# Kernel tuning notes

Hardware: AMD Instinct MI355X
Metric: run time of the kernel (lower is better)

Reference implementation:

```python
import jax, jax.numpy as jnp
import numpy as np

B, N, K = 2, 8192, 16
C_IN, C_OUT = 32, 64
EPS = 1e-6


def _bn(x, g, b, axes):
    m = jnp.mean(x, axes, keepdims=True)
    v = jnp.var(x, axes, keepdims=True)
    return (x - m) * jax.lax.rsqrt(v + EPS) * g + b


def _leaky(x, s):
    return jnp.where(x >= 0, x, s * x)


def _knn(coords, k):
    # brute-force euclidean KNN, self point included (dist 0)
    sq = jnp.sum(coords * coords, -1)  # (B,N)
    d2 = sq[:, :, None] + sq[:, None, :] - 2.0 * jnp.einsum('bnd,bmd->bnm', coords, coords)
    neg, idx = jax.lax.top_k(-d2, k)  # (B,N,K)
    dist = jnp.sqrt(jnp.clip(-neg, 1e-12, None))
    return idx, dist


def setup_inputs() -> dict:
    key = jax.random.key(0)
    ks = jax.random.split(key, 12)
    h = C_OUT // 2
    w = lambda k, s: jax.random.normal(k, s, jnp.float32) * 0.05
    return {
        'coords': jax.random.normal(ks[0], (B, N, 3), jnp.float32),
        'features': jax.random.normal(ks[1], (B, N, C_IN), jnp.float32),
        'W_mlp1': w(ks[2], (C_IN, h)), 'b_mlp1': jnp.zeros(h, jnp.float32),
        'W_lse1': w(ks[3], (10, h)), 'b_lse1': jnp.zeros(h, jnp.float32),
        'g_lse1': jnp.ones(h, jnp.float32), 'be_lse1': jnp.zeros(h, jnp.float32),
        'W_att1_lin': w(ks[4], (C_OUT, C_OUT)),
        'W_att1_mlp': w(ks[5], (C_OUT, h)), 'b_att1_mlp': jnp.zeros(h, jnp.float32),
        'g_att1': jnp.ones(h, jnp.float32), 'be_att1': jnp.zeros(h, jnp.float32),
        'W_lse2': w(ks[6], (10, h)), 'b_lse2': jnp.zeros(h, jnp.float32),
        'g_lse2': jnp.ones(h, jnp.float32), 'be_lse2': jnp.zeros(h, jnp.float32),
        'W_att2_lin': w(ks[7], (C_OUT, C_OUT)),
        'W_att2_mlp': w(ks[8], (C_OUT, C_OUT)), 'b_att2_mlp': jnp.zeros(C_OUT, jnp.float32),
        'g_att2': jnp.ones(C_OUT, jnp.float32), 'be_att2': jnp.zeros(C_OUT, jnp.float32),
        'W_mlp2': w(ks[9], (C_OUT, 2 * C_OUT)), 'b_mlp2': jnp.zeros(2 * C_OUT, jnp.float32),
        'W_short': w(ks[10], (C_IN, 2 * C_OUT)), 'b_short': jnp.zeros(2 * C_OUT, jnp.float32),
        'g_short': jnp.ones(2 * C_OUT, jnp.float32), 'be_short': jnp.zeros(2 * C_OUT, jnp.float32),
    }


def _forward(coords, features, W_mlp1, b_mlp1, W_lse1, b_lse1, g_lse1, be_lse1,
             W_att1_lin, W_att1_mlp, b_att1_mlp, g_att1, be_att1,
             W_lse2, b_lse2, g_lse2, be_lse2,
             W_att2_lin, W_att2_mlp, b_att2_mlp, g_att2, be_att2,
             W_mlp2, b_mlp2, W_short, b_short, g_short, be_short):
    idx, dist = _knn(coords, K)                     # (B,N,K)
    nbr = jax.vmap(lambda c, i: c[i])(coords, idx)  # gather neighbor coords (B,N,K,3)
    center = jnp.broadcast_to(coords[:, :, None, :], nbr.shape)
    # spatial encoding: [center, neighbor, center-neighbor, dist] -> 10 channels
    se = jnp.concatenate([center, nbr, center - nbr, dist[..., None]], -1)  # (B,N,K,10)

    # mlp1 (1x1 conv + LeakyReLU(0.2)), no BN
    x = _leaky(features @ W_mlp1 + b_mlp1, 0.2)     # (B,N,h)

    # LocSE 1: shared MLP (BN train-mode + ReLU) on spatial enc, concat features
    sp1 = jax.nn.relu(_bn(se @ W_lse1 + b_lse1, g_lse1, be_lse1, (0, 1, 2)))  # (B,N,K,h)
    x1 = jnp.concatenate([sp1, jnp.broadcast_to(x[:, :, None, :], sp1.shape)], -1)  # (B,N,K,2h)

    # attention pooling 1: softmax over neighbors K, weighted sum, MLP+BN+ReLU
    sc1 = jax.nn.softmax(x1 @ W_att1_lin, axis=2)
    p1 = jnp.sum(sc1 * x1, axis=2)                  # (B,N,2h)
    x = jax.nn.relu(_bn(p1 @ W_att1_mlp + b_att1_mlp, g_att1, be_att1, (0, 1)))  # (B,N,h)

    # LocSE 2 + attention pooling 2 (same KNN, separate weights)
    sp2 = jax.nn.relu(_bn(se @ W_lse2 + b_lse2, g_lse2, be_lse2, (0, 1, 2)))
    x2 = jnp.concatenate([sp2, jnp.broadcast_to(x[:, :, None, :], sp2.shape)], -1)
    sc2 = jax.nn.softmax(x2 @ W_att2_lin, axis=2)
    p2 = jnp.sum(sc2 * x2, axis=2)
    x = jax.nn.relu(_bn(p2 @ W_att2_mlp + b_att2_mlp, g_att2, be_att2, (0, 1)))  # (B,N,C_OUT)

    # mlp2 (no BN, no act) + shortcut (BN, no act), residual LeakyReLU(0.01)
    x = x @ W_mlp2 + b_mlp2                          # (B,N,2*C_OUT)
    short = _bn(features @ W_short + b_short, g_short, be_short, (0, 1))
    out = _leaky(x + short, 0.01)
    # match torch layout (B, 2*C_OUT, N, 1)
    return jnp.transpose(out, (0, 2, 1))[..., None]


def reference(coords, features, W_mlp1, b_mlp1, W_lse1, b_lse1, g_lse1, be_lse1,
              W_att1_lin, W_att1_mlp, b_att1_mlp, g_att1, be_att1,
              W_lse2, b_lse2, g_lse2, be_lse2,
              W_att2_lin, W_att2_mlp, b_att2_mlp, g_att2, be_att2,
              W_mlp2, b_mlp2, W_short, b_short, g_short, be_short):
    return _forward(coords, features, W_mlp1, b_mlp1, W_lse1, b_lse1, g_lse1, be_lse1,
                    W_att1_lin, W_att1_mlp, b_att1_mlp, g_att1, be_att1,
                    W_lse2, b_lse2, g_lse2, be_lse2,
                    W_att2_lin, W_att2_mlp, b_att2_mlp, g_att2, be_att2,
                    W_mlp2, b_mlp2, W_short, b_short, g_short, be_short)
```

## Files before the change

### kernel.cpp

```cpp
#include <hip/hip_runtime.h>
#include <cfloat>
#include <cmath>

#define DEV __device__ __forceinline__

constexpr int BB = 2, NN = 8192, KK = 16, CIN = 32, HH = 32, CO = 64, C2 = 128;
constexpr int BNTOT = BB * NN;
constexpr int BNKROWS = BB * NN * KK;
constexpr float EPSF = 1e-6f;
constexpr int NCELL = 4096;
constexpr int CAP = 128;

constexpr int S_LSE1 = 0, S_LSE2 = 64, S_ATT1 = 128, S_ATT2 = 192, S_SHORT = 320, S_TOTAL = 576;

constexpr size_t OFF_CP4   = 0;
constexpr size_t OFF_SE    = OFF_CP4 + (size_t)BNTOT * 4;
constexpr size_t OFF_XF    = OFF_SE + (size_t)BNKROWS * 10;
constexpr size_t OFF_SHORT = OFF_XF + (size_t)BNTOT * HH;
constexpr size_t OFF_PRE1  = OFF_SHORT + (size_t)BNTOT * C2;
constexpr size_t OFF_PRE2  = OFF_PRE1 + (size_t)BNTOT * HH;
constexpr size_t OFF_STATS = OFF_PRE2 + (size_t)BNTOT * CO;
constexpr size_t OFF_COUNTS= OFF_STATS + 2 * S_TOTAL;
constexpr size_t OFF_TB    = OFF_COUNTS + 2 * NCELL;
constexpr size_t OFF_CODE  = OFF_SHORT;
constexpr size_t OFF_CPS   = OFF_CODE + 16384;
constexpr size_t OFF_OIDX  = OFF_CPS + (size_t)BNTOT * 4 + 16;

DEV unsigned spr3(unsigned v) {
    return (v & 1u) | ((v & 2u) << 2) | ((v & 4u) << 4) | ((v & 8u) << 6);
}

__global__ __launch_bounds__(256) void k_prep(const float* __restrict__ coords,
                                              float4* __restrict__ cp4,
                                              int* __restrict__ code, int* __restrict__ counts) {
#pragma clang fp contract(off)
    int i = blockIdx.x * 256 + threadIdx.x;
    if (i >= BNTOT) return;
    float x = coords[3 * i], y = coords[3 * i + 1], z = coords[3 * i + 2];
    float sq = (x * x + y * y) + z * z;
    cp4[i] = make_float4(x, y, z, sq);
    const float inv = 16.f / 8.8f;
    int ix = min(15, max(0, (int)floorf((x + 4.4f) * inv)));
    int iy = min(15, max(0, (int)floorf((y + 4.4f) * inv)));
    int iz = min(15, max(0, (int)floorf((z + 4.4f) * inv)));
    unsigned m = spr3(ix) | (spr3(iy) << 1) | (spr3(iz) << 2);
    code[i] = (int)m;
    atomicAdd(&counts[((i >> 13) << 12) + m], 1);
}

__global__ __launch_bounds__(256) void k_scan(int* __restrict__ counts) {
    __shared__ int lds[256];
    int t = threadIdx.x;
    int base = blockIdx.x * NCELL;
    int v[16]; int s = 0;
#pragma unroll
    for (int k = 0; k < 16; ++k) { int tmp = counts[base + t * 16 + k]; v[k] = s; s += tmp; }
    lds[t] = s;
    __syncthreads();
    for (int o = 1; o < 256; o <<= 1) {
        int u = (t >= o) ? lds[t - o] : 0;
        __syncthreads();
        lds[t] += u;
        __syncthreads();
    }
    int off = lds[t] - s;
#pragma unroll
    for (int k = 0; k < 16; ++k) counts[base + t * 16 + k] = off + v[k];
}

__global__ __launch_bounds__(256) void k_scatter(const float4* __restrict__ cp4,
                                                 const int* __restrict__ code,
                                                 int* __restrict__ cursor,
                                                 float4* __restrict__ cps, int* __restrict__ oidx) {
    int i = blockIdx.x * 256 + threadIdx.x;
    if (i >= BNTOT) return;
    int b = i >> 13, n = i & 8191;
    int c = code[i];
    int pos = atomicAdd(&cursor[(b << 12) + c], 1);
    cps[(b << 13) + pos] = cp4[i];
    oidx[(b << 13) + pos] = n;
}

DEV float dist2(float4 qc, float4 c) {
#pragma clang fp contract(off)
    float dot = (qc.x * c.x + qc.y * c.y) + qc.z * c.z;
    return (qc.w + c.w) - 2.0f * dot;
}

DEV void insv16(float (&dl)[16], float d) {
    float dk = d;
#pragma unroll
    for (int r = 0; r < 16; ++r) {
        bool c = dk < dl[r];
        float td = dl[r];
        dl[r] = c ? dk : dl[r];
        dk = c ? td : dk;
    }
}

DEV void ins16_lex(float (&dl)[16], int (&il)[16], float d, int id) {
    float dk = d; int jk = id;
#pragma unroll
    for (int r = 0; r < 16; ++r) {
        bool c = (dk < dl[r]) || (dk == dl[r] && jk < il[r]);
        float td = dl[r]; int ti = il[r];
        dl[r] = c ? dk : dl[r]; il[r] = c ? jk : il[r];
        dk = c ? td : dk; jk = c ? ti : jk;
    }
}

__global__ __launch_bounds__(256) void k_seed(const float4* __restrict__ cps,
                                              const int* __restrict__ oidx,
                                              float* __restrict__ tbound) {
    int t = threadIdx.x;
    int ql = t >> 2, sub = t & 3;
    int b = blockIdx.x >> 7;
    int p = ((blockIdx.x & 127) << 6) + ql;
    const float4* cb_ = cps + ((size_t)b << 13);
    float4 qc = cb_[p];
    int s = p - 128;
    s = s < 0 ? 0 : (s > NN - 256 ? NN - 256 : s);
    s += sub * 64;
    float dl[16];
#pragma unroll
    for (int i = 0; i < 16; ++i) dl[i] = FLT_MAX;
    for (int j = 0; j < 64; j += 4) {
        float4 c0 = cb_[s + j], c1 = cb_[s + j + 1], c2 = cb_[s + j + 2], c3 = cb_[s + j + 3];
        float d0 = dist2(qc, c0), d1 = dist2(qc, c1), d2v = dist2(qc, c2), d3 = dist2(qc, c3);
        if (d0 < dl[15]) insv16(dl, d0);
        if (d1 < dl[15]) insv16(dl, d1);
        if (d2v < dl[15]) insv16(dl, d2v);
        if (d3 < dl[15]) insv16(dl, d3);
    }
#pragma unroll
    for (int o = 1; o < 4; o <<= 1) {
        float dd[16];
#pragma unroll
        for (int i = 0; i < 16; ++i) dd[i] = __shfl_xor(dl[i], o);
#pragma unroll
        for (int i = 0; i < 16; ++i) if (dd[i] < dl[15]) insv16(dl, dd[i]);
    }
    if (sub == 0) tbound[(b << 13) + oidx[(b << 13) + p]] = dl[15];
}

__global__ __launch_bounds__(256) void k_knn(const float4* __restrict__ cp4,
                                             const float* __restrict__ tbound,
                                             float* __restrict__ se) {
    __shared__ __align__(16) float4 tile[1024];
    __shared__ uint2 surv[16][CAP + 1];
    __shared__ int scnt[16];
    __shared__ float sd[16][17];
    __shared__ int   si[16][17];
    __shared__ int nof;
    __shared__ float t2s;

    int t = threadIdx.x;
    int b = blockIdx.x >> 9;
    int qbase = (blockIdx.x & 511) * 16;
    int ql = t & 15, part = t >> 4;
    int wv = t >> 6, lane = t & 63;
    const float4* cp = cp4 + ((size_t)b << 13);
    int q = qbase + ql;
    float4 qc = cp[q];
    float T = tbound[(b << 13) + q];

    if (t < 16) scnt[t] = 0;

    float4 r0 = cp[t], r1 = cp[t + 256], r2 = cp[t + 512], r3 = cp[t + 768];

    for (int tb = 0; tb < 8192; tb += 1024) {
        __syncthreads();
        tile[t] = r0; tile[t + 256] = r1; tile[t + 512] = r2; tile[t + 768] = r3;
        if (tb + 1024 < 8192) {
            const float4* nx = cp + tb + 1024;
            r0 = nx[t]; r1 = nx[t + 256]; r2 = nx[t + 512]; r3 = nx[t + 768];
        }
        __syncthreads();
        for (int j = 0; j < 64; j += 4) {
            float4 c0 = tile[part + 16 * j];
            float4 c1 = tile[part + 16 * (j + 1)];
            float4 c2 = tile[part + 16 * (j + 2)];
            float4 c3 = tile[part + 16 * (j + 3)];
            float d0 = dist2(qc, c0), d1 = dist2(qc, c1), d2v = dist2(qc, c2), d3 = dist2(qc, c3);
            bool p0 = d0 <= T, p1 = d1 <= T, p2 = d2v <= T, p3 = d3 <= T;
            if (__any(p0 | p1 | p2 | p3)) {
                int jb = tb + part;
                if (p0) { int pos = atomicAdd(&scnt[ql], 1); if (pos < CAP) surv[ql][pos] = make_uint2(__float_as_uint(d0), (unsigned)(jb + 16 * j)); }
                if (p1) { int pos = atomicAdd(&scnt[ql], 1); if (pos < CAP) surv[ql][pos] = make_uint2(__float_as_uint(d1), (unsigned)(jb + 16 * (j + 1))); }
                if (p2) { int pos = atomicAdd(&scnt[ql], 1); if (pos < CAP) surv[ql][pos] = make_uint2(__float_as_uint(d2v), (unsigned)(jb + 16 * (j + 2))); }
                if (p3) { int pos = atomicAdd(&scnt[ql], 1); if (pos < CAP) surv[ql][pos] = make_uint2(__float_as_uint(d3), (unsigned)(jb + 16 * (j + 3))); }
            }
        }
    }
    __syncthreads();

    for (int rpass = 0; rpass < 3; ++rpass) {
        if (t == 0) nof = 0;
        __syncthreads();
        if (t < 16 && scnt[t] > CAP) atomicAdd(&nof, 1);
        __syncthreads();
        if (!nof) break;
        for (int q2 = 0; q2 < 16; ++q2) {
            int n0 = scnt[q2];
            __syncthreads();
            if (n0 <= CAP) continue;
            if (t == 0) {
                float dl[16];
#pragma unroll
                for (int i = 0; i < 16; ++i) dl[i] = FLT_MAX;
                for (int s2 = 0; s2 < CAP; ++s2) {
                    float d = __uint_as_float(surv[q2][s2].x);
                    if (d < dl[15]) insv16(dl, d);
                }
                t2s = dl[15];
                scnt[q2] = 0;
            }
            __syncthreads();
            float T2 = t2s;
            float4 qc2 = cp[qbase + q2];
            int jb = t * 32;
            for (int j = jb; j < jb + 32; j += 4) {
                float4 c0 = cp[j], c1 = cp[j + 1], c2 = cp[j + 2], c3 = cp[j + 3];
                float d0 = dist2(qc2, c0), d1 = dist2(qc2, c1), d2v = dist2(qc2, c2), d3 = dist2(qc2, c3);
                if (d0 <= T2) { int pos = atomicAdd(&scnt[q2], 1); if (pos < CAP) surv[q2][pos] = make_uint2(__float_as_uint(d0), (unsigned)j); }
                if (d1 <= T2) { int pos = atomicAdd(&scnt[q2], 1); if (pos < CAP) surv[q2][pos] = make_uint2(__float_as_uint(d1), (unsigned)(j + 1)); }
                if (d2v <= T2) { int pos = atomicAdd(&scnt[q2], 1); if (pos < CAP) surv[q2][pos] = make_uint2(__float_as_uint(d2v), (unsigned)(j + 2)); }
                if (d3 <= T2) { int pos = atomicAdd(&scnt[q2], 1); if (pos < CAP) surv[q2][pos] = make_uint2(__float_as_uint(d3), (unsigned)(j + 3)); }
            }
            __syncthreads();
        }
    }

    for (int q2 = wv; q2 < 16; q2 += 4) {
        if (scnt[q2] > CAP) {
            float4 qc2 = cp[qbase + q2];
            float dl[16]; int il[16];
#pragma unroll
            for (int i = 0; i < 16; ++i) { dl[i] = FLT_MAX; il[i] = 0x7fffffff; }
            for (int i = 0; i < 128; ++i) {
                int j = lane + (i << 6);
                float d = dist2(qc2, cp[j]);
                if (d < dl[15] || (d == dl[15] && j < il[15])) ins16_lex(dl, il, d, j);
            }
            for (int o = 1; o < 64; o <<= 1) {
                float dd[16]; int ii[16];
#pragma unroll
                for (int i = 0; i < 16; ++i) { dd[i] = __shfl_xor(dl[i], o); ii[i] = __shfl_xor(il[i], o); }
#pragma unroll
                for (int i = 0; i < 16; ++i) {
                    if (dd[i] < dl[15] || (dd[i] == dl[15] && ii[i] < il[15])) ins16_lex(dl, il, dd[i], ii[i]);
                }
            }
            if (lane == 0) {
#pragma unroll
                for (int i = 0; i < 16; ++i) { sd[q2][i] = dl[i]; si[q2][i] = il[i]; }
            }
        }
    }

    if (t < 16 && scnt[t] <= CAP) {
        int n = scnt[t];
        float dl[16]; int il[16];
#pragma unroll
        for (int i = 0; i < 16; ++i) { dl[i] = FLT_MAX; il[i] = 0x7fffffff; }
        for (int s2 = 0; s2 < n; ++s2) {
            uint2 v = surv[t][s2];
            float d = __uint_as_float(v.x); int id = (int)v.y;
            if (d < dl[15] || (d == dl[15] && id < il[15])) ins16_lex(dl, il, d, id);
        }
#pragma unroll
        for (int i = 0; i < 16; ++i) { sd[t][i] = dl[i]; si[t][i] = il[i]; }
    }
    __syncthreads();

    {
        int qq = t >> 4, k = t & 15;
        float d2s = sd[qq][k]; int id = si[qq][k];
        float4 qc2 = cp[qbase + qq];
        float4 nb = cp[id];
        float dist = sqrtf(fmaxf(d2s, 1e-12f));
        float* sp = se + ((size_t)(b * NN + qbase + qq) * KK + k) * 10;
        sp[0] = qc2.x; sp[1] = qc2.y; sp[2] = qc2.z;
        sp[3] = nb.x;  sp[4] = nb.y;  sp[5] = nb.z;
        sp[6] = qc2.x - nb.x; sp[7] = qc2.y - nb.y; sp[8] = qc2.z - nb.z;
        sp[9] = dist;
    }
}

__global__ __launch_bounds__(128) void k_feat(const float* __restrict__ feat,
                                              const float* __restrict__ Wm1, const float* __restrict__ bm1,
                                              const float* __restrict__ Wsh, const float* __restrict__ bsh,
                                              float* __restrict__ xf, float* __restrict__ short_pre,
                                              double* __restrict__ stats) {
    __shared__ float fl[32][33];
    int t = threadIdx.x;
    int pbase = blockIdx.x * 32;
    float wcol[32];
#pragma unroll
    for (int i = 0; i < 32; ++i) wcol[i] = Wsh[i * C2 + t];
    float wm[32];
    if (t < 32) {
#pragma unroll
        for (int i = 0; i < 32; ++i) wm[i] = Wm1[i * HH + t];
    }
    float bs = bsh[t];
    float bm = (t < 32) ? bm1[t] : 0.f;
    double s = 0.0, s2 = 0.0;

    for (int e = t; e < 1024; e += 128) {
        int p = e >> 5, i = e & 31;
        fl[p][i] = feat[(size_t)(pbase + p) * CIN + i];
    }
    __syncthreads();
    for (int p = 0; p < 32; ++p) {
        float acc = bs;
#pragma unroll
        for (int i = 0; i < 32; ++i) acc += fl[p][i] * wcol[i];
        int gp = pbase + p;
        short_pre[(size_t)gp * C2 + t] = acc;
        s += acc; s2 += (double)acc * acc;
        if (t < 32) {
            float xv = bm;
#pragma unroll
            for (int i = 0; i < 32; ++i) xv += fl[p][i] * wm[i];
            xf[(size_t)gp * HH + t] = xv >= 0.f ? xv : 0.2f * xv;
        }
    }
    atomicAdd(&stats[S_SHORT + t], s);
    atomicAdd(&stats[S_SHORT + C2 + t], s2);
}

__global__ __launch_bounds__(256) void k_lse_stats(const float* __restrict__ se,
                                                   const float* __restrict__ W1, const float* __restrict__ b1,
                                                   const float* __restrict__ W2, const float* __restrict__ b2,
                                                   double* __restrict__ stats) {
    __shared__ float srows[256][10];
    __shared__ double red[4][64][2];
    int t = threadIdx.x;
    int c = t & 63, grp = t >> 6;
    int ch = c & 31; bool second = c >= 32;
    const float* W = second ? W2 : W1;
    float wcol[10];
#pragma unroll
    for (int d = 0; d < 10; ++d) wcol[d] = W[d * HH + ch];
    float bb = second ? b2[ch] : b1[ch];
    double s = 0.0, s2 = 0.0;
    int rbase = blockIdx.x * 512;

    for (int tile = 0; tile < 2; ++tile) {
        __syncthreads();
        const float* src = se + (size_t)(rbase + tile * 256) * 10;
        for (int e = t; e < 2560; e += 256) srows[e / 10][e % 10] = src[e];
        __syncthreads();
        int r0 = grp * 64;
        for (int r = r0; r < r0 + 64; ++r) {
            float acc = bb;
#pragma unroll
            for (int d = 0; d < 10; ++d) acc += srows[r][d] * wcol[d];
            s += acc; s2 += (double)acc * acc;
        }
    }
    red[grp][c][0] = s; red[grp][c][1] = s2;
    __syncthreads();
    if (grp == 0) {
        for (int g = 1; g < 4; ++g) { s += red[g][c][0]; s2 += red[g][c][1]; }
        int base = second ? S_LSE2 : S_LSE1;
        atomicAdd(&stats[base + ch], s);
        atomicAdd(&stats[base + 32 + ch], s2);
    }
}

DEV float2 fin_pair(const double* stats, int sbase, int ch, int nch, double M,
                    const float* g, const float* be) {
    double mean = stats[sbase + ch] / M;
    double var = stats[sbase + nch + ch] / M - mean * mean;
    double scd = (double)g[ch] / sqrt(var + (double)EPSF);
    return make_float2((float)scd, (float)((double)be[ch] - mean * scd));
}

template <int OUTC, bool SECOND>
__global__ __launch_bounds__(256) void k_att(const float* __restrict__ se,
                                             const float* __restrict__ featsrc,
                                             const float* __restrict__ Wlse, const float* __restrict__ blse,
                                             const float* __restrict__ Wlin,
                                             const float* __restrict__ Wmlp, const float* __restrict__ bmlp,
                                             double* __restrict__ stats, int lse_sbase, int feat_sbase, int stat_base,
                                             const float* __restrict__ g_lse, const float* __restrict__ be_lse,
                                             const float* __restrict__ g_f, const float* __restrict__ be_f,
                                             float* __restrict__ preout) {
    __shared__ __align__(16) float wlt[64][68];
    __shared__ float wm[64][OUTC];
    __shared__ __align__(16) float x1[4][16][40];
    __shared__ float fv[4][32];
    __shared__ float p1b[4][64];
    __shared__ double red[4][OUTC][2];

    int t = threadIdx.x, w = t >> 6, c = t & 63;
    int ch = c & 31, half = c >> 5;
    for (int e = t; e < 4096; e += 256) wlt[e & 63][e >> 6] = Wlin[e];
    for (int e = t; e < 64 * OUTC; e += 256) wm[e / OUTC][e % OUTC] = Wmlp[e];

    float wf[10]; float bf;
    {
        float2 p = fin_pair(stats, lse_sbase, ch, 32, (double)BNKROWS, g_lse, be_lse);
#pragma unroll
        for (int d = 0; d < 10; ++d) wf[d] = Wlse[d * 32 + ch] * p.x;
        bf = blse[ch] * p.x + p.y;
    }
    float fa = 1.f, fb = 0.f;
    if (SECOND && c >= 32) {
        float2 p = fin_pair(stats, feat_sbase, ch, 32, (double)BNTOT, g_f, be_f);
        fa = p.x; fb = p.y;
    }
    double s = 0.0, s2 = 0.0;
    __syncthreads();

    for (int i = 0; i < 4; ++i) {
        int p = blockIdx.x * 16 + w * 4 + i;

        int kbase = half * 8;
        const float* sp = se + (size_t)p * (KK * 10) + kbase * 10;
        float myv[8];
#pragma unroll
        for (int kk = 0; kk < 8; ++kk) {
            float acc = bf;
#pragma unroll
            for (int d = 0; d < 10; ++d) acc += sp[kk * 10 + d] * wf[d];
            myv[kk] = fmaxf(acc, 0.f);
        }
#pragma unroll
        for (int kk = 0; kk < 8; ++kk) x1[w][kbase + kk][ch] = myv[kk];

        float xv = 0.f;
        if (c >= 32) {
            xv = featsrc[(size_t)p * 32 + ch];
            if (SECOND) xv = fmaxf(xv * fa + fb, 0.f);
            fv[w][ch] = xv;
        }

        float col[16];
        if (c < 32) {
#pragma unroll
            for (int kk = 0; kk < 8; ++kk) col[kk] = myv[kk];
#pragma unroll
            for (int kk = 0; kk < 8; ++kk) col[8 + kk] = x1[w][8 + kk][ch];
        } else {
#pragma unroll
            for (int k = 0; k < 16; ++k) col[k] = xv;
        }

        float cst = 0.f;
#pragma unroll
        for (int dg = 8; dg < 16; ++dg) {
            float4 wv = *(const float4*)&wlt[c][dg * 4];
            float4 xvv = *(const float4*)&fv[w][(dg - 8) * 4];
            cst += xvv.x * wv.x + xvv.y * wv.y + xvv.z * wv.z + xvv.w * wv.w;
        }
        float scv[16];
#pragma unroll
        for (int k = 0; k < 16; ++k) scv[k] = cst;
        for (int dg = 0; dg < 8; ++dg) {
            float4 wv = *(const float4*)&wlt[c][dg * 4];
#pragma unroll
            for (int k = 0; k < 16; ++k) {
                float4 xvv = *(const float4*)&x1[w][k][dg * 4];
                scv[k] += xvv.x * wv.x + xvv.y * wv.y + xvv.z * wv.z + xvv.w * wv.w;
            }
        }
        float m = scv[0];
#pragma unroll
        for (int k = 1; k < 16; ++k) m = fmaxf(m, scv[k]);
        float sum = 0.f, p1 = 0.f;
#pragma unroll
        for (int k = 0; k < 16; ++k) { float e = __expf(scv[k] - m); sum += e; p1 += e * col[k]; }
        p1 /= sum;
        p1b[w][c] = p1;

        if (c < OUTC) {
            float acc = bmlp[c];
#pragma unroll
            for (int d = 0; d < 64; ++d) acc += p1b[w][d] * wm[d][c];
            preout[(size_t)p * OUTC + c] = acc;
            s += acc; s2 += (double)acc * acc;
        }
    }
    if (c < OUTC) { red[w][c][0] = s; red[w][c][1] = s2; }
    __syncthreads();
    if (t < OUTC) {
        double ts = red[0][t][0], ts2 = red[0][t][1];
        for (int g = 1; g < 4; ++g) { ts += red[g][t][0]; ts2 += red[g][t][1]; }
        atomicAdd(&stats[stat_base + t], ts);
        atomicAdd(&stats[stat_base + OUTC + t], ts2);
    }
}

__global__ __launch_bounds__(256) void k_out(const float* __restrict__ pre2,
                                             const float* __restrict__ short_pre,
                                             const float* __restrict__ W2, const float* __restrict__ b2,
                                             const double* __restrict__ stats,
                                             const float* __restrict__ g_a2, const float* __restrict__ be_a2,
                                             const float* __restrict__ g_s, const float* __restrict__ be_s,
                                             float* __restrict__ out) {
    __shared__ __align__(16) float w2[64][128];
    __shared__ float sc2[64], sh2[64], scs[128], shs[128], bb[128];
    int t = threadIdx.x;
    int pl = t & 31, seg = t >> 5;
    for (int e = t; e < 8192; e += 256) w2[e >> 7][e & 127] = W2[e];
    if (t < 64) { float2 p = fin_pair(stats, S_ATT2, t, 64, (double)BNTOT, g_a2, be_a2); sc2[t] = p.x; sh2[t] = p.y; }
    if (t >= 64 && t < 192) { int ch = t - 64; float2 p = fin_pair(stats, S_SHORT, ch, 128, (double)BNTOT, g_s, be_s); scs[ch] = p.x; shs[ch] = p.y; }
    if (t < 128) bb[t] = b2[t];
    __syncthreads();

    int p = blockIdx.x * 32 + pl;
    int b = p >> 13, n = p & 8191;
    const float* pr = pre2 + (size_t)p * 64;
    float xa[64];
#pragma unroll
    for (int c = 0; c < 64; c += 4) {
        float4 v = *(const float4*)&pr[c];
        xa[c + 0] = fmaxf(v.x * sc2[c + 0] + sh2[c + 0], 0.f);
        xa[c + 1] = fmaxf(v.y * sc2[c + 1] + sh2[c + 1], 0.f);
        xa[c + 2] = fmaxf(v.z * sc2[c + 2] + sh2[c + 2], 0.f);
        xa[c + 3] = fmaxf(v.w * sc2[c + 3] + sh2[c + 3], 0.f);
    }
    const float* shp = short_pre + (size_t)p * 128;
    int obase = seg * 16;
    for (int o = obase; o < obase + 16; o += 4) {
        float a0 = bb[o], a1 = bb[o + 1], a2 = bb[o + 2], a3 = bb[o + 3];
#pragma unroll
        for (int cc = 0; cc < 64; ++cc) {
            float4 wv = *(const float4*)&w2[cc][o];
            float x = xa[cc];
            a0 += x * wv.x; a1 += x * wv.y; a2 += x * wv.z; a3 += x * wv.w;
        }
        float4 sv = *(const float4*)&shp[o];
        float r0 = a0 + (sv.x * scs[o] + shs[o]);
        float r1 = a1 + (sv.y * scs[o + 1] + shs[o + 1]);
        float r2 = a2 + (sv.z * scs[o + 2] + shs[o + 2]);
        float r3 = a3 + (sv.w * scs[o + 3] + shs[o + 3]);
        out[((size_t)(b * C2 + o + 0)) * NN + n] = r0 >= 0.f ? r0 : 0.01f * r0;
        out[((size_t)(b * C2 + o + 1)) * NN + n] = r1 >= 0.f ? r1 : 0.01f * r1;
        out[((size_t)(b * C2 + o + 2)) * NN + n] = r2 >= 0.f ? r2 : 0.01f * r2;
        out[((size_t)(b * C2 + o + 3)) * NN + n] = r3 >= 0.f ? r3 : 0.01f * r3;
    }
}

extern "C" void kernel_launch(void* const* d_in, const int* in_sizes, int n_in,
                              void* d_out, int out_size, void* d_ws, size_t ws_size,
                              hipStream_t stream) {
    const float* coords    = (const float*)d_in[0];
    const float* features  = (const float*)d_in[1];
    const float* W_mlp1    = (const float*)d_in[2];
    const float* b_mlp1    = (const float*)d_in[3];
    const float* W_lse1    = (const float*)d_in[4];
    const float* b_lse1    = (const float*)d_in[5];
    const float* g_lse1    = (const float*)d_in[6];
    const float* be_lse1   = (const float*)d_in[7];
    const float* W_att1_lin= (const float*)d_in[8];
    const float* W_att1_mlp= (const float*)d_in[9];
    const float* b_att1_mlp= (const float*)d_in[10];
    const float* g_att1    = (const float*)d_in[11];
    const float* be_att1   = (const float*)d_in[12];
    const float* W_lse2    = (const float*)d_in[13];
    const float* b_lse2    = (const float*)d_in[14];
    const float* g_lse2    = (const float*)d_in[15];
    const float* be_lse2   = (const float*)d_in[16];
    const float* W_att2_lin= (const float*)d_in[17];
    const float* W_att2_mlp= (const float*)d_in[18];
    const float* b_att2_mlp= (const float*)d_in[19];
    const float* g_att2    = (const float*)d_in[20];
    const float* be_att2   = (const float*)d_in[21];
    const float* W_mlp2    = (const float*)d_in[22];
    const float* b_mlp2    = (const float*)d_in[23];
    const float* W_short   = (const float*)d_in[24];
    const float* b_short   = (const float*)d_in[25];
    const float* g_short   = (const float*)d_in[26];
    const float* be_short  = (const float*)d_in[27];

    float* ws = (float*)d_ws;
    float4* cp4      = (float4*)(ws + OFF_CP4);
    float* se        = ws + OFF_SE;
    float* xf        = ws + OFF_XF;
    float* short_pre = ws + OFF_SHORT;
    float* pre1      = ws + OFF_PRE1;
    float* pre2      = ws + OFF_PRE2;
    double* stats    = (double*)(ws + OFF_STATS);
    int* counts      = (int*)(ws + OFF_COUNTS);
    float* tbound    = ws + OFF_TB;
    int* code        = (int*)(ws + OFF_CODE);
    float4* cps      = (float4*)(ws + OFF_CPS);
    int* oidxArr     = (int*)(ws + OFF_OIDX);
    float* out       = (float*)d_out;

    hipMemsetAsync(stats, 0, S_TOTAL * 8 + 2 * NCELL * 4, stream);

    k_prep<<<BNTOT / 256, 256, 0, stream>>>(coords, cp4, code, counts);
    k_scan<<<2, 256, 0, stream>>>(counts);
    k_scatter<<<BNTOT / 256, 256, 0, stream>>>(cp4, code, counts, cps, oidxArr);
    k_seed<<<BNTOT / 64, 256, 0, stream>>>(cps, oidxArr, tbound);
    k_knn<<<1024, 256, 0, stream>>>(cp4, tbound, se);
    k_feat<<<512, 128, 0, stream>>>(features, W_mlp1, b_mlp1, W_short, b_short,
                                    xf, short_pre, stats);
    k_lse_stats<<<512, 256, 0, stream>>>(se, W_lse1, b_lse1, W_lse2, b_lse2, stats);
    k_att<32, false><<<1024, 256, 0, stream>>>(se, xf, W_lse1, b_lse1, W_att1_lin,
                                               W_att1_mlp, b_att1_mlp, stats,
                                               S_LSE1, 0, S_ATT1,
                                               g_lse1, be_lse1, nullptr, nullptr, pre1);
    k_att<64, true><<<1024, 256, 0, stream>>>(se, pre1, W_lse2, b_lse2, W_att2_lin,
                                              W_att2_mlp, b_att2_mlp, stats,
                                              S_LSE2, S_ATT1, S_ATT2,
                                              g_lse2, be_lse2, g_att1, be_att1, pre2);
    k_out<<<BNTOT / 32, 256, 0, stream>>>(pre2, short_pre, W_mlp2, b_mlp2, stats,
                                          g_att2, be_att2, g_short, be_short, out);
}
```

Before: 393.5 us.

## Prune KNN candidate chunks using per-chunk bounding boxes in spatially sorted order

Adds a kernel that computes a bounding box for each 64-point chunk of the Morton-sorted point array. Each KNN block then processes its 16 queries in sorted order, keeps only the chunks whose box lies within the largest seed bound of the block's query box, and streams just those chunks through shared memory. The aim is to avoid brute-force distance evaluation against all 8192 points. The cost is an extra small launch, an indirect index lookup for surviving candidates, a scatter of outputs back to original order, and reliance on a small epsilon margin for correctness.

New measurement: 501.0 us. +27.3%, slower.

```diff
diff --git a/kernel.cpp b/kernel.cpp
--- a/kernel.cpp
+++ b/kernel.cpp
@@ -25,6 +25,7 @@
 constexpr size_t OFF_CODE  = OFF_SHORT;
 constexpr size_t OFF_CPS   = OFF_CODE + 16384;
 constexpr size_t OFF_OIDX  = OFF_CPS + (size_t)BNTOT * 4 + 16;
+constexpr size_t OFF_BBOX  = OFF_OIDX + 16384;
 
 DEV unsigned spr3(unsigned v) {
     return (v & 1u) | ((v & 2u) << 2) | ((v & 4u) << 4) | ((v & 8u) << 6);
@@ -81,6 +82,22 @@
     oidx[(b << 13) + pos] = n;
 }
 
+__global__ __launch_bounds__(64) void k_bbox(const float4* __restrict__ cps,
+                                             float* __restrict__ bboxg) {
+    int c = blockIdx.x, lane = threadIdx.x;
+    float4 p = cps[c * 64 + lane];
+    float lox = p.x, hix = p.x, loy = p.y, hiy = p.y, loz = p.z, hiz = p.z;
+    for (int o = 32; o > 0; o >>= 1) {
+        lox = fminf(lox, __shfl_down(lox, o)); hix = fmaxf(hix, __shfl_down(hix, o));
+        loy = fminf(loy, __shfl_down(loy, o)); hiy = fmaxf(hiy, __shfl_down(hiy, o));
+        loz = fminf(loz, __shfl_down(loz, o)); hiz = fmaxf(hiz, __shfl_down(hiz, o));
+    }
+    if (lane == 0) {
+        float* bb = bboxg + c * 8;
+        bb[0] = lox; bb[1] = loy; bb[2] = loz; bb[3] = hix; bb[4] = hiy; bb[5] = hiz;
+    }
+}
+
 DEV float dist2(float4 qc, float4 c) {
 #pragma clang fp contract(off)
     float dot = (qc.x * c.x + qc.y * c.y) + qc.z * c.z;
@@ -110,7 +127,6 @@
 }
 
 __global__ __launch_bounds__(256) void k_seed(const float4* __restrict__ cps,
-                                              const int* __restrict__ oidx,
                                               float* __restrict__ tbound) {
     int t = threadIdx.x;
     int ql = t >> 2, sub = t & 3;
@@ -140,10 +156,13 @@
 #pragma unroll
         for (int i = 0; i < 16; ++i) if (dd[i] < dl[15]) insv16(dl, dd[i]);
     }
-    if (sub == 0) tbound[(b << 13) + oidx[(b << 13) + p]] = dl[15];
-}
-
-__global__ __launch_bounds__(256) void k_knn(const float4* __restrict__ cp4,
+    if (sub == 0) tbound[(b << 13) + p] = dl[15];
+}
+
+__global__ __launch_bounds__(256) void k_knn(const float4* __restrict__ cps,
+                                             const int* __restrict__ oidx,
+                                             const float4* __restrict__ cp4,
+                                             const float* __restrict__ bboxg,
                                              const float* __restrict__ tbound,
                                              float* __restrict__ se) {
     __shared__ __align__(16) float4 tile[1024];
@@ -153,42 +172,86 @@
     __shared__ int   si[16][17];
     __shared__ int nof;
     __shared__ float t2s;
+    __shared__ float qx[16], qy[16], qz[16], Tarr[16];
+    __shared__ int clist[128];
+    __shared__ int ccnt;
 
     int t = threadIdx.x;
     int b = blockIdx.x >> 9;
     int qbase = (blockIdx.x & 511) * 16;
     int ql = t & 15, part = t >> 4;
     int wv = t >> 6, lane = t & 63;
-    const float4* cp = cp4 + ((size_t)b << 13);
+    const float4* cb_ = cps + ((size_t)b << 13);
+    const int* ob_ = oidx + (b << 13);
+    const float4* cpo = cp4 + ((size_t)b << 13);
+    const float* bbase = bboxg + (b << 10);
     int q = qbase + ql;
-    float4 qc = cp[q];
+    float4 qc = cb_[q];
     float T = tbound[(b << 13) + q];
 
-    if (t < 16) scnt[t] = 0;
-
-    float4 r0 = cp[t], r1 = cp[t + 256], r2 = cp[t + 512], r3 = cp[t + 768];
-
-    for (int tb = 0; tb < 8192; tb += 1024) {
+    if (t < 16) {
+        scnt[t] = 0;
+        qx[t] = qc.x; qy[t] = qc.y; qz[t] = qc.z; Tarr[t] = T;
+    }
+    if (t == 16) ccnt = 0;
+    __syncthreads();
+
+    if (t < 128) {
+        float gxl = qx[0], gxh = qx[0], gyl = qy[0], gyh = qy[0], gzl = qz[0], gzh = qz[0], Tm = Tarr[0];
+#pragma unroll
+        for (int i = 1; i < 16; ++i) {
+            gxl = fminf(gxl, qx[i]); gxh = fmaxf(gxh, qx[i]);
+            gyl = fminf(gyl, qy[i]); gyh = fmaxf(gyh, qy[i]);
+            gzl = fminf(gzl, qz[i]); gzh = fmaxf(gzh, qz[i]);
+            Tm = fmaxf(Tm, Tarr[i]);
+        }
+        const float* bp = bbase + t * 8;
+        float dx = fmaxf(0.f, fmaxf(bp[0] - gxh, gxl - bp[3]));
+        float dy = fmaxf(0.f, fmaxf(bp[1] - gyh, gyl - bp[4]));
+        float dz = fmaxf(0.f, fmaxf(bp[2] - gzh, gzl - bp[5]));
+        float md2 = dx * dx + dy * dy + dz * dz;
+        if (md2 <= Tm * 1.001f + 1e-3f) {
+            int p2 = atomicAdd(&ccnt, 1);
+            clist[p2] = t;
+        }
+    }
+    __syncthreads();
+    int C = ccnt;
+    int nt = (C + 15) >> 4;
+
+    float4 r0, r1, r2, r3;
+    {
+        int e0 = t, e1 = t + 256, e2 = t + 512, e3 = t + 768;
+        int c0 = clist[min(e0 >> 6, C - 1)], c1 = clist[min(e1 >> 6, C - 1)];
+        int c2 = clist[min(e2 >> 6, C - 1)], c3 = clist[min(e3 >> 6, C - 1)];
+        r0 = cb_[c0 * 64 + (e0 & 63)]; r1 = cb_[c1 * 64 + (e1 & 63)];
+        r2 = cb_[c2 * 64 + (e2 & 63)]; r3 = cb_[c3 * 64 + (e3 & 63)];
+    }
+
+    for (int ti = 0; ti < nt; ++ti) {
         __syncthreads();
         tile[t] = r0; tile[t + 256] = r1; tile[t + 512] = r2; tile[t + 768] = r3;
-        if (tb + 1024 < 8192) {
-            const float4* nx = cp + tb + 1024;
-            r0 = nx[t]; r1 = nx[t + 256]; r2 = nx[t + 512]; r3 = nx[t + 768];
-        }
-        __syncthreads();
-        for (int j = 0; j < 64; j += 4) {
-            float4 c0 = tile[part + 16 * j];
-            float4 c1 = tile[part + 16 * (j + 1)];
-            float4 c2 = tile[part + 16 * (j + 2)];
-            float4 c3 = tile[part + 16 * (j + 3)];
+        if (ti + 1 < nt) {
+            int base = (ti + 1) * 16;
+            int e0 = t, e1 = t + 256, e2 = t + 512, e3 = t + 768;
+            int c0 = clist[min(base + (e0 >> 6), C - 1)], c1 = clist[min(base + (e1 >> 6), C - 1)];
+            int c2 = clist[min(base + (e2 >> 6), C - 1)], c3 = clist[min(base + (e3 >> 6), C - 1)];
+            r0 = cb_[c0 * 64 + (e0 & 63)]; r1 = cb_[c1 * 64 + (e1 & 63)];
+            r2 = cb_[c2 * 64 + (e2 & 63)]; r3 = cb_[c3 * 64 + (e3 & 63)];
+        }
+        __syncthreads();
+        int Ct = min(16, C - ti * 16);
+        for (int j = 0; j < 4 * Ct; j += 4) {
+            int s0 = part + 16 * j, s1 = s0 + 16, s2c = s0 + 32, s3 = s0 + 48;
+            float4 c0 = tile[s0], c1 = tile[s1], c2 = tile[s2c], c3 = tile[s3];
             float d0 = dist2(qc, c0), d1 = dist2(qc, c1), d2v = dist2(qc, c2), d3 = dist2(qc, c3);
             bool p0 = d0 <= T, p1 = d1 <= T, p2 = d2v <= T, p3 = d3 <= T;
             if (__any(p0 | p1 | p2 | p3)) {
-                int jb = tb + part;
-                if (p0) { int pos = atomicAdd(&scnt[ql], 1); if (pos < CAP) surv[ql][pos] = make_uint2(__float_as_uint(d0), (unsigned)(jb + 16 * j)); }
-                if (p1) { int pos = atomicAdd(&scnt[ql], 1); if (pos < CAP) surv[ql][pos] = make_uint2(__float_as_uint(d1), (unsigned)(jb + 16 * (j + 1))); }
-                if (p2) { int pos = atomicAdd(&scnt[ql], 1); if (pos < CAP) surv[ql][pos] = make_uint2(__float_as_uint(d2v), (unsigned)(jb + 16 * (j + 2))); }
-                if (p3) { int pos = atomicAdd(&scnt[ql], 1); if (pos < CAP) surv[ql][pos] = make_uint2(__float_as_uint(d3), (unsigned)(jb + 16 * (j + 3))); }
+                int lb = ti * 16;
+                if (p0) { int js = clist[lb + (s0 >> 6)] * 64 + (s0 & 63); int pos = atomicAdd(&scnt[ql], 1); if (pos < CAP) surv[ql][pos] = make_uint2(__float_as_uint(d0), (unsigned)ob_[js]); }
+                if (p1) { int js = clist[lb + (s1 >> 6)] * 64 + (s1 & 63); int pos = atomicAdd(&scnt[ql], 1); if (pos < CAP) surv[ql][pos] = make_uint2(__float_as_uint(d1), (unsigned)ob_[js]); }
+                if (p2) { int js = clist[lb + (s2c >> 6)] * 64 + (s2c & 63); int pos = atomicAdd(&scnt[ql], 1); if (pos < CAP) surv[ql][pos] = make_uint2(__float_as_uint(d2v), (unsigned)ob_[js]); }
+                if (p3) { int js = clist[lb + (s3 >> 6)] * 64 + (s3 & 63); int pos = atomicAdd(&scnt[ql], 1); if (pos < CAP) surv[ql][pos] = make_uint2(__float_as_uint(d3), (unsigned)ob_[js]); }
             }
         }
     }
@@ -217,10 +280,10 @@
             }
             __syncthreads();
             float T2 = t2s;
-            float4 qc2 = cp[qbase + q2];
+            float4 qc2 = cb_[qbase + q2];
             int jb = t * 32;
             for (int j = jb; j < jb + 32; j += 4) {
-                float4 c0 = cp[j], c1 = cp[j + 1], c2 = cp[j + 2], c3 = cp[j + 3];
+                float4 c0 = cpo[j], c1 = cpo[j + 1], c2 = cpo[j + 2], c3 = cpo[j + 3];
                 float d0 = dist2(qc2, c0), d1 = dist2(qc2, c1), d2v = dist2(qc2, c2), d3 = dist2(qc2, c3);
                 if (d0 <= T2) { int pos = atomicAdd(&scnt[q2], 1); if (pos < CAP) surv[q2][pos] = make_uint2(__float_as_uint(d0), (unsigned)j); }
                 if (d1 <= T2) { int pos = atomicAdd(&scnt[q2], 1); if (pos < CAP) surv[q2][pos] = make_uint2(__float_as_uint(d1), (unsigned)(j + 1)); }
@@ -233,13 +296,13 @@
 
     for (int q2 = wv; q2 < 16; q2 += 4) {
         if (scnt[q2] > CAP) {
-            float4 qc2 = cp[qbase + q2];
+            float4 qc2 = cb_[qbase + q2];
             float dl[16]; int il[16];
 #pragma unroll
             for (int i = 0; i < 16; ++i) { dl[i] = FLT_MAX; il[i] = 0x7fffffff; }
             for (int i = 0; i < 128; ++i) {
                 int j = lane + (i << 6);
-                float d = dist2(qc2, cp[j]);
+                float d = dist2(qc2, cpo[j]);
                 if (d < dl[15] || (d == dl[15] && j < il[15])) ins16_lex(dl, il, d, j);
             }
             for (int o = 1; o < 64; o <<= 1) {
@@ -275,11 +338,12 @@
 
     {
         int qq = t >> 4, k = t & 15;
-        float d2s = sd[qq][k]; int id = si[qq][k];
-        float4 qc2 = cp[qbase + qq];
-        float4 nb = cp[id];
+        float d2s = sd[qq][k]; int oid = si[qq][k];
+        float4 qc2 = cb_[qbase + qq];
+        int oq = ob_[qbase + qq];
+        float4 nb = cpo[oid];
         float dist = sqrtf(fmaxf(d2s, 1e-12f));
-        float* sp = se + ((size_t)(b * NN + qbase + qq) * KK + k) * 10;
+        float* sp = se + ((size_t)(b * NN + oq) * KK + k) * 10;
         sp[0] = qc2.x; sp[1] = qc2.y; sp[2] = qc2.z;
         sp[3] = nb.x;  sp[4] = nb.y;  sp[5] = nb.z;
         sp[6] = qc2.x - nb.x; sp[7] = qc2.y - nb.y; sp[8] = qc2.z - nb.z;
@@ -590,6 +654,7 @@
     int* code        = (int*)(ws + OFF_CODE);
     float4* cps      = (float4*)(ws + OFF_CPS);
     int* oidxArr     = (int*)(ws + OFF_OIDX);
+    float* bboxg     = ws + OFF_BBOX;
     float* out       = (float*)d_out;
 
     hipMemsetAsync(stats, 0, S_TOTAL * 8 + 2 * NCELL * 4, stream);
@@ -597,8 +662,9 @@
     k_prep<<<BNTOT / 256, 256, 0, stream>>>(coords, cp4, code, counts);
     k_scan<<<2, 256, 0, stream>>>(counts);
     k_scatter<<<BNTOT / 256, 256, 0, stream>>>(cp4, code, counts, cps, oidxArr);
-    k_seed<<<BNTOT / 64, 256, 0, stream>>>(cps, oidxArr, tbound);
-    k_knn<<<1024, 256, 0, stream>>>(cp4, tbound, se);
+    k_bbox<<<BB * 128, 64, 0, stream>>>(cps, bboxg);
+    k_seed<<<BNTOT / 64, 256, 0, stream>>>(cps, tbound);
+    k_knn<<<1024, 256, 0, stream>>>(cps, oidxArr, cp4, bboxg, tbound, se);
     k_feat<<<512, 128, 0, stream>>>(features, W_mlp1, b_mlp1, W_short, b_short,
                                     xf, short_pre, stats);
     k_lse_stats<<<512, 256, 0, stream>>>(se, W_lse1, b_lse1, W_lse2, b_lse2, stats);
```
